# Kernel tuning notes

Measured on AMD Instinct MI355X. Metric: run time of the kernel, lower is better.

## Reference

```python
import jax, jax.numpy as jnp
import numpy as np

B, V, T, P, F, H = 256, 16, 64, 24, 8, 256
OUT = 4  # output_size


def setup_inputs() -> dict:
    key = jax.random.key(0)
    ks = jax.random.split(key, 8)
    s = 0.1
    return {
        "sequence": jax.random.uniform(ks[0], (B, V, T, F), dtype=jnp.float32),
        "dist_matrix": jax.random.uniform(ks[1], (B, V, V), dtype=jnp.float32),
        "rb_matrix": jax.random.uniform(ks[2], (B, V, V), dtype=jnp.float32),
        "cog_matrix": jax.random.uniform(ks[3], (B, V, V), dtype=jnp.float32),
        "seq_mask": jnp.ones((B, V, T), dtype=jnp.float32),
        "maxval": jnp.ones((B, F), dtype=jnp.float32),
        "minval": jnp.zeros((B, F), dtype=jnp.float32),
        # per-vessel distinct LSTMCell weights (torch gate order i,f,g,o)
        "W_ih": jax.random.normal(ks[4], (V, 4 * H, F), dtype=jnp.float32) * s,
        "W_hh": jax.random.normal(ks[5], (V, 4 * H, H), dtype=jnp.float32) * s,
        "b_ih": jnp.zeros((V, 4 * H), dtype=jnp.float32),
        "b_hh": jnp.zeros((V, 4 * H), dtype=jnp.float32),
        # per-vessel attention Linear(2H -> H)
        "W_att": jax.random.normal(ks[6], (V, H, 2 * H), dtype=jnp.float32) * s,
        "b_att": jnp.zeros((V, H), dtype=jnp.float32),
        # shared output Linear(H -> F)
        "W_out": jax.random.normal(ks[7], (F, H), dtype=jnp.float32) * s,
        "b_out": jnp.zeros((F,), dtype=jnp.float32),
        "maxVessels": V,
    }


def _lstm(x, h, c, W_ih, W_hh, b_ih, b_hh):
    # grouped LSTMCell over all vessels at once: x [B,V,F], h/c [B,V,H]
    gates = (jnp.einsum('bvf,vgf->bvg', x, W_ih) + b_ih
             + jnp.einsum('bvh,vgh->bvg', h, W_hh) + b_hh)
    i, f, g, o = jnp.split(gates, 4, axis=-1)
    c = jax.nn.sigmoid(f) * c + jax.nn.sigmoid(i) * jnp.tanh(g)
    h = jax.nn.sigmoid(o) * jnp.tanh(c)
    return h, c


def reference(sequence, dist_matrix, rb_matrix, cog_matrix, seq_mask, maxval, minval,
              W_ih, W_hh, b_ih, b_hh, W_att, b_att, W_out, b_out, maxVessels):
    B_, V_, T_, F_ = sequence.shape
    H_ = W_hh.shape[-1]
    mx = maxval[:, None, :]  # [B,1,F] -> broadcast to [B,V,F]
    mn = minval[:, None, :]

    # ---- encoder: scan over sequence_length, all vessels batched ----
    def enc_step(carry, x_t):
        h, c = carry
        h, c = _lstm(x_t, h, c, W_ih, W_hh, b_ih, b_hh)
        return (h, c), h

    h0 = jnp.zeros((B_, V_, H_), sequence.dtype)
    c0 = jnp.zeros((B_, V_, H_), sequence.dtype)
    (h, c), enc = jax.lax.scan(enc_step, (h0, c0), jnp.moveaxis(sequence, 2, 0))
    enc = jnp.moveaxis(enc, 0, 2)  # [B,V,T,H]

    # ---- decoder: scan over prediction_length ----
    def dec_step(carry, _):
        h, c, prev = carry
        # torch.tensor(x.data) detaches -> stop_gradient; then denormalize
        prev_seq = jax.lax.stop_gradient(prev) * (mx - mn) + mn
        # attention score: batched dot of encoder states with decoder hidden
        score = jnp.einsum('bvth,bvh->bvt', enc, h)
        alpha = jax.nn.softmax(score * seq_mask, axis=-1)
        cv = jnp.einsum('bvt,bvth->bvh', alpha, enc)  # context vector
        # faithful replication of torch.stack((cv, h)).view(B, 2H) per vessel
        cat = jnp.stack([cv, h], axis=0)              # [2,B,V,H]
        cat = cat.transpose(2, 0, 1, 3).reshape(V_, B_, 2 * H_)  # [V,B,2H]
        h_att = jnp.tanh(jnp.einsum('vbk,vhk->vbh', cat, W_att) + b_att[:, None, :])
        h_att = h_att.transpose(1, 0, 2)              # [B,V,H]
        h2, c2 = _lstm(prev_seq, h_att, c, W_ih, W_hh, b_ih, b_hh)
        out = jax.nn.relu(jnp.einsum('bvh,fh->bvf', h2, W_out) + b_out)
        return (h2, c2, out), out

    prev0 = sequence[:, :, -1, :]
    _, outs = jax.lax.scan(dec_step, (h, c, prev0), None, length=P)
    outs = jnp.moveaxis(outs, 0, 2)  # [B,V,P,F]
    return jnp.clip(outs[..., :OUT], 0.0, 1.0)
```

## Files before the change

kernel.cpp:

```cpp
#include <hip/hip_runtime.h>
#include <hip/hip_bf16.h>

namespace {

typedef unsigned short u16;
constexpr int B_ = 256, V_ = 16, T_ = 64, P_ = 24, F_ = 8, H_ = 256, G_ = 1024;

typedef __attribute__((ext_vector_type(8))) short bf16x8;
typedef __attribute__((ext_vector_type(4))) float f32x4;

__device__ __forceinline__ float sigm(float x) { return 1.0f / (1.0f + __expf(-x)); }
__device__ __forceinline__ float bf2f(u16 s) {
  union { unsigned u; float f; } x; x.u = ((unsigned)s) << 16; return x.f;
}
__device__ __forceinline__ u16 f2bf(float f) {
  union { float f; unsigned u; } x; x.f = f;
  unsigned r = x.u + 0x7fffu + ((x.u >> 16) & 1u);
  return (u16)(r >> 16);
}
__device__ __forceinline__ void split2(float w, u16& hi, u16& lo) {
  hi = f2bf(w);
  lo = f2bf(w - bf2f(hi));
}
__device__ __forceinline__ void load16(const void* g, void* l) {
  __builtin_amdgcn_global_load_lds(
      (const __attribute__((address_space(1))) unsigned*)g,
      (__attribute__((address_space(3))) unsigned*)l, 16, 0, 0);
}
__device__ __forceinline__ f32x4 mfma16(bf16x8 a, bf16x8 b, f32x4 c) {
  return __builtin_amdgcn_mfma_f32_16x16x32_bf16(a, b, c, 0, 0, 0);
}

__global__ void init_kernel(float* __restrict__ c, float* __restrict__ prev,
                            const float* __restrict__ seq) {
  int idx = blockIdx.x * 256 + threadIdx.x;
  if (idx < B_ * V_ * H_ / 4) ((float4*)c)[idx] = float4{0.f, 0.f, 0.f, 0.f};
  if (idx < B_ * V_ * F_ / 4) {
    int v = idx >> 9, rem = idx & 511;
    int b = rem >> 1, fq = rem & 1;
    ((float4*)prev)[idx] = ((const float4*)seq)[(((size_t)b * V_ + v) * T_ + (T_ - 1)) * 2 + fq];
  }
}

__global__ void convert_kernel(const float* __restrict__ Whh, const float* __restrict__ Watt,
                               u16* __restrict__ whhH, u16* __restrict__ whhL,
                               u16* __restrict__ wattH, u16* __restrict__ wattL) {
  int gid = blockIdx.x * 256 + threadIdx.x;
  const int n1 = V_ * G_ * H_ / 4;
  const int n2 = V_ * H_ * 2 * H_ / 4;
  const float* src; u16 *dH, *dL; int i;
  if (gid < n1)            { src = Whh;  dH = whhH;  dL = whhL;  i = gid; }
  else if (gid < n1 + n2)  { src = Watt; dH = wattH; dL = wattL; i = gid - n1; }
  else return;
  float4 wv = ((const float4*)src)[i];
  u16 h0,l0,h1,l1,h2,l2,h3,l3;
  split2(wv.x,h0,l0); split2(wv.y,h1,l1); split2(wv.z,h2,l2); split2(wv.w,h3,l3);
  uint2 oh; oh.x = (unsigned)h0 | ((unsigned)h1 << 16); oh.y = (unsigned)h2 | ((unsigned)h3 << 16);
  uint2 ol; ol.x = (unsigned)l0 | ((unsigned)l1 << 16); ol.y = (unsigned)l2 | ((unsigned)l3 << 16);
  ((uint2*)dH)[i] = oh; ((uint2*)dL)[i] = ol;
}

__global__ void copy_h_kernel(const u16* __restrict__ enc, const u16* __restrict__ hlo1,
                              u16* __restrict__ hdecHi, u16* __restrict__ hdecLo) {
  int gid = blockIdx.x * 256 + threadIdx.x;
  int row = gid >> 5, jq = gid & 31;
  ((uint4*)hdecHi)[gid] = ((const uint4*)enc)[((size_t)row * T_ + (T_ - 1)) * 32 + jq];
  ((uint4*)hdecLo)[gid] = ((const uint4*)hlo1)[gid];
}

template <int MODE>
__global__ __launch_bounds__(512) void lstm_mfma_kernel(
    const float* __restrict__ xin,
    u16* __restrict__ enc,
    const u16* __restrict__ hloIn,
    u16* __restrict__ hloOut,
    const u16* __restrict__ aHi,
    const u16* __restrict__ aLo,
    u16* __restrict__ hdecHi, u16* __restrict__ hdecLo,
    float* __restrict__ cbuf,
    const u16* __restrict__ WhhHi, const u16* __restrict__ WhhLo,
    const float* __restrict__ W_ih, const float* __restrict__ b_ih,
    const float* __restrict__ b_hh,
    const float* __restrict__ maxv, const float* __restrict__ minv,
    int t)
{
  __shared__ char smem[74240];
  float* xsf   = (float*)(smem + 65536);
  float* wisf  = (float*)(smem + 69632);
  float* bsumf = (float*)(smem + 73728);

  int bid = blockIdx.x;
  int xcd = bid & 7, idx = bid >> 3;
  int v  = xcd * 2 + (idx & 1);
  int bt = (idx >> 1) & 1;
  int ch = idx >> 2;
  int b0 = bt * 128, c0 = ch * 32;
  int tid = threadIdx.x, lane = tid & 63, w = tid >> 6;
  int wr = w >> 1, wc = w & 1;

  if (tid < 256) {
    int b_l = tid >> 1, fq = tid & 1;
    int b = b0 + b_l;
    float4 xv;
    if (MODE == 0) {
      xv = *(const float4*)(xin + (((size_t)b * V_ + v) * T_ + t) * F_ + fq * 4);
    } else {
      float4 pv = *(const float4*)(xin + ((size_t)v * B_ + b) * F_ + fq * 4);
      float4 mx = *(const float4*)(maxv + b * F_ + fq * 4);
      float4 mn = *(const float4*)(minv + b * F_ + fq * 4);
      xv.x = pv.x * (mx.x - mn.x) + mn.x;
      xv.y = pv.y * (mx.y - mn.y) + mn.y;
      xv.z = pv.z * (mx.z - mn.z) + mn.z;
      xv.w = pv.w * (mx.w - mn.w) + mn.w;
    }
    *(float4*)(xsf + b_l * 8 + fq * 4) = xv;
  } else {
    int idx2 = tid - 256;
    int gc = idx2 >> 1, half = idx2 & 1;
    int grow = ((gc >> 5) << 8) + c0 + (gc & 31);
    *(float4*)(wisf + gc * 8 + half * 4) =
        *(const float4*)(W_ih + ((size_t)v * G_ + grow) * F_ + half * 4);
  }
  if (tid < 128) {
    int grow = ((tid >> 5) << 8) + c0 + (tid & 31);
    bsumf[tid] = b_ih[v * G_ + grow] + b_hh[v * G_ + grow];
  }

  const bool hasK = (MODE == 1) || (t > 0);

  auto stageAB = [&](int ks, int bufn) {
    int kc = ks * 32;
    int row = tid >> 2, g2 = tid & 3;
    int kb = ((g2 ^ ((row >> 1) & 3)) << 4);
    size_t boff = ((((size_t)v * G_ + ((row >> 5) << 8) + c0 + (row & 31)) * H_ + kc) << 1) + kb;
    load16((const char*)WhhHi + boff, smem + 32768 + bufn * 8192 + tid * 16);
    load16((const char*)WhhLo + boff, smem + 49152 + bufn * 8192 + tid * 16);
    if (MODE == 0) {
      size_t offH = ((((size_t)(v * B_ + b0 + row)) * T_ + (t - 1)) * H_ + kc) * 2 + kb;
      size_t offL = (((size_t)(v * B_ + b0 + row)) * H_ + kc) * 2 + kb;
      load16((const char*)enc + offH,   smem + bufn * 8192 + tid * 16);
      load16((const char*)hloIn + offL, smem + 16384 + bufn * 8192 + tid * 16);
    } else {
      size_t offA = (((size_t)(v * B_ + b0 + row)) * H_ + kc) * 2 + kb;
      load16((const char*)aHi + offA, smem + bufn * 8192 + tid * 16);
      load16((const char*)aLo + offA, smem + 16384 + bufn * 8192 + tid * 16);
    }
  };

  f32x4 acc[2][4];
  #pragma unroll
  for (int i = 0; i < 2; ++i)
    #pragma unroll
    for (int g = 0; g < 4; ++g) acc[i][g] = f32x4{0.f, 0.f, 0.f, 0.f};

  if (hasK) stageAB(0, 0);
  __syncthreads();

  if (hasK) {
    int rA = lane & 15, kg = lane >> 4;
    int ar0 = wr * 32 + rA;
    int aoff0 = ar0 * 64 + ((kg ^ ((ar0 >> 1) & 3)) << 4);
    int br0 = wc * 16 + rA;
    int boff0 = br0 * 64 + ((kg ^ ((br0 >> 1) & 3)) << 4);
    int buf = 0;
    for (int ks = 0; ks < 8; ++ks) {
      if (ks < 7) stageAB(ks + 1, buf ^ 1);
      const char* Ah = smem + buf * 8192;
      const char* Al = smem + 16384 + buf * 8192;
      const char* Bh = smem + 32768 + buf * 8192;
      const char* Bl = smem + 49152 + buf * 8192;
      bf16x8 ah0 = *(const bf16x8*)(Ah + aoff0);
      bf16x8 ah1 = *(const bf16x8*)(Ah + aoff0 + 1024);
      bf16x8 al0 = *(const bf16x8*)(Al + aoff0);
      bf16x8 al1 = *(const bf16x8*)(Al + aoff0 + 1024);
      bf16x8 bh[4], bl[4];
      #pragma unroll
      for (int g = 0; g < 4; ++g) {
        bh[g] = *(const bf16x8*)(Bh + boff0 + g * 2048);
        bl[g] = *(const bf16x8*)(Bl + boff0 + g * 2048);
      }
      #pragma unroll
      for (int g = 0; g < 4; ++g) {
        acc[0][g] = mfma16(ah0, bh[g], acc[0][g]);
        acc[1][g] = mfma16(ah1, bh[g], acc[1][g]);
      }
      #pragma unroll
      for (int g = 0; g < 4; ++g) {
        acc[0][g] = mfma16(al0, bh[g], acc[0][g]);
        acc[1][g] = mfma16(al1, bh[g], acc[1][g]);
      }
      #pragma unroll
      for (int g = 0; g < 4; ++g) {
        acc[0][g] = mfma16(ah0, bl[g], acc[0][g]);
        acc[1][g] = mfma16(ah1, bl[g], acc[1][g]);
      }
      __syncthreads();
      buf ^= 1;
    }
  }

  {
    int rA = lane & 15;
    int cc = wc * 16 + rA;
    int col = c0 + cc;
    float bs[4], wr8[4][8];
    #pragma unroll
    for (int g = 0; g < 4; ++g) {
      int gc = g * 32 + cc;
      bs[g] = bsumf[gc];
      #pragma unroll
      for (int f = 0; f < 8; ++f) wr8[g][f] = wisf[gc * 8 + f];
    }
    int rowg = (lane >> 4) * 4;
    #pragma unroll
    for (int i = 0; i < 2; ++i) {
      #pragma unroll
      for (int r = 0; r < 4; ++r) {
        int b_l = wr * 32 + i * 16 + rowg + r;
        const float* xf = xsf + b_l * 8;
        float s[4];
        #pragma unroll
        for (int g = 0; g < 4; ++g) {
          float sv = acc[i][g][r] + bs[g];
          #pragma unroll
          for (int f = 0; f < 8; ++f) sv = fmaf(wr8[g][f], xf[f], sv);
          s[g] = sv;
        }
        size_t gidx = ((size_t)(v * B_ + b0 + b_l)) * H_ + col;
        float cold = cbuf[gidx];
        float cn = sigm(s[1]) * cold + sigm(s[0]) * tanhf(s[2]);
        float hn = sigm(s[3]) * tanhf(cn);
        cbuf[gidx] = cn;
        u16 hi, lo; split2(hn, hi, lo);
        if (MODE == 0) {
          enc[(((size_t)(v * B_ + b0 + b_l)) * T_ + t) * H_ + col] = hi;
          hloOut[gidx] = lo;
        } else {
          hdecHi[gidx] = hi;
          hdecLo[gidx] = lo;
        }
      }
    }
  }
}

__global__ __launch_bounds__(256) void attn_kernel(
    const u16* __restrict__ enc, const u16* __restrict__ hHi, const u16* __restrict__ hLo,
    const float* __restrict__ mask, u16* __restrict__ cvHi, u16* __restrict__ cvLo)
{
  __shared__ u16 et[T_ * H_];
  __shared__ float hh[H_];
  __shared__ float ss[T_];
  int bx = blockIdx.x;
  int v = bx >> 8, b = bx & 255;
  int tid = threadIdx.x;

  const char* erow = (const char*)(enc + ((size_t)(v * B_ + b)) * T_ * H_);
  #pragma unroll
  for (int it2 = 0; it2 < 8; ++it2) {
    int gidx = it2 * 256 + tid;
    load16(erow + gidx * 16, (char*)et + gidx * 16);
  }
  {
    size_t hidx = ((size_t)v * B_ + b) * H_ + tid;
    hh[tid] = bf2f(hHi[hidx]) + bf2f(hLo[hidx]);
  }
  __syncthreads();

  int t = tid >> 2, part = tid & 3;
  const u16* ep = et + t * H_ + part * 64;
  float acc = 0.f;
  #pragma unroll
  for (int it = 0; it < 8; ++it) {
    uint4 uu = *(const uint4*)(ep + it * 8);
    const float* hp = &hh[part * 64 + it * 8];
    acc = fmaf(bf2f((u16)(uu.x & 0xffff)), hp[0], acc);
    acc = fmaf(bf2f((u16)(uu.x >> 16)),    hp[1], acc);
    acc = fmaf(bf2f((u16)(uu.y & 0xffff)), hp[2], acc);
    acc = fmaf(bf2f((u16)(uu.y >> 16)),    hp[3], acc);
    acc = fmaf(bf2f((u16)(uu.z & 0xffff)), hp[4], acc);
    acc = fmaf(bf2f((u16)(uu.z >> 16)),    hp[5], acc);
    acc = fmaf(bf2f((u16)(uu.w & 0xffff)), hp[6], acc);
    acc = fmaf(bf2f((u16)(uu.w >> 16)),    hp[7], acc);
  }
  acc += __shfl_xor(acc, 1, 64);
  acc += __shfl_xor(acc, 2, 64);
  if (part == 0) ss[t] = acc * mask[((size_t)b * V_ + v) * T_ + t];
  __syncthreads();

  if (tid < 64) {
    float s = ss[tid];
    float m = s;
    #pragma unroll
    for (int d = 32; d >= 1; d >>= 1) m = fmaxf(m, __shfl_xor(m, d, 64));
    float e = __expf(s - m);
    float se = e;
    #pragma unroll
    for (int d = 32; d >= 1; d >>= 1) se += __shfl_xor(se, d, 64);
    ss[tid] = e / se;
  }
  __syncthreads();

  int j = tid;
  float a = 0.f;
  #pragma unroll 8
  for (int tt = 0; tt < T_; ++tt)
    a = fmaf(ss[tt], bf2f(et[tt * H_ + j]), a);
  u16 hi, lo; split2(a, hi, lo);
  size_t cidx = ((size_t)v * B_ + b) * H_ + j;
  cvHi[cidx] = hi;
  cvLo[cidx] = lo;
}

__global__ __launch_bounds__(256) void attg_mfma_kernel(
    const u16* __restrict__ cvHi, const u16* __restrict__ cvLo,
    const u16* __restrict__ hdHi, const u16* __restrict__ hdLo,
    const u16* __restrict__ WattHi, const u16* __restrict__ WattLo,
    const float* __restrict__ b_att,
    u16* __restrict__ hattHi, u16* __restrict__ hattLo)
{
  __shared__ char smem[40960];
  int bx = blockIdx.x;
  int v = bx >> 4, bt = (bx >> 1) & 7, nh = bx & 1;
  int bp0 = bt * 32, n0 = nh * 128;
  int tid = threadIdx.x, lane = tid & 63, w = tid >> 6;

  auto stageAB = [&](int ks, int bufn) {
    int kc = ks * 32;
    #pragma unroll
    for (int it = 0; it < 2; ++it) {
      int gb = it * 256 + tid;
      int nl = gb >> 2, g2 = gb & 3;
      int kb = ((g2 ^ ((nl >> 1) & 3)) << 4);
      size_t off = ((((size_t)v * H_ + n0 + nl) * (2 * H_) + kc) << 1) + kb;
      load16((const char*)WattHi + off, smem + 8192  + bufn * 8192 + gb * 16);
      load16((const char*)WattLo + off, smem + 24576 + bufn * 8192 + gb * 16);
    }
    {
      int g = tid & 127;
      int b = g >> 2, g2 = g & 3;
      int kb = ((g2 ^ ((b >> 1) & 3)) << 4);
      int bp = bp0 + b;
      const u16* baseH = (bp < 128) ? (cvHi + ((size_t)v * B_ + 2 * bp) * H_)
                                    : (hdHi + ((size_t)v * B_ + 2 * (bp - 128)) * H_);
      const u16* baseL = (bp < 128) ? (cvLo + ((size_t)v * B_ + 2 * bp) * H_)
                                    : (hdLo + ((size_t)v * B_ + 2 * (bp - 128)) * H_);
      if (tid < 128) load16((const char*)baseH + kc * 2 + kb, smem + bufn * 2048 + g * 16);
      else           load16((const char*)baseL + kc * 2 + kb, smem + 4096 + bufn * 2048 + g * 16);
    }
  };

  f32x4 acc[2][2];
  #pragma unroll
  for (int i = 0; i < 2; ++i)
    #pragma unroll
    for (int j = 0; j < 2; ++j) acc[i][j] = f32x4{0.f, 0.f, 0.f, 0.f};

  stageAB(0, 0);
  __syncthreads();

  int rA = lane & 15, kg = lane >> 4;
  int aoff0 = rA * 64 + ((kg ^ ((rA >> 1) & 3)) << 4);
  int gc0 = w * 32 + rA;
  int boff0 = gc0 * 64 + ((kg ^ ((gc0 >> 1) & 3)) << 4);
  int buf = 0;
  for (int ks = 0; ks < 16; ++ks) {
    if (ks < 15) stageAB(ks + 1, buf ^ 1);
    const char* Ah = smem + buf * 2048;
    const char* Al = smem + 4096  + buf * 2048;
    const char* Bh = smem + 8192  + buf * 8192;
    const char* Bl = smem + 24576 + buf * 8192;
    bf16x8 ah0 = *(const bf16x8*)(Ah + aoff0);
    bf16x8 ah1 = *(const bf16x8*)(Ah + aoff0 + 1024);
    bf16x8 al0 = *(const bf16x8*)(Al + aoff0);
    bf16x8 al1 = *(const bf16x8*)(Al + aoff0 + 1024);
    bf16x8 bh0 = *(const bf16x8*)(Bh + boff0);
    bf16x8 bh1 = *(const bf16x8*)(Bh + boff0 + 1024);
    bf16x8 bl0 = *(const bf16x8*)(Bl + boff0);
    bf16x8 bl1 = *(const bf16x8*)(Bl + boff0 + 1024);
    acc[0][0] = mfma16(ah0, bh0, acc[0][0]);
    acc[0][1] = mfma16(ah0, bh1, acc[0][1]);
    acc[1][0] = mfma16(ah1, bh0, acc[1][0]);
    acc[1][1] = mfma16(ah1, bh1, acc[1][1]);
    acc[0][0] = mfma16(al0, bh0, acc[0][0]);
    acc[0][1] = mfma16(al0, bh1, acc[0][1]);
    acc[1][0] = mfma16(al1, bh0, acc[1][0]);
    acc[1][1] = mfma16(al1, bh1, acc[1][1]);
    acc[0][0] = mfma16(ah0, bl0, acc[0][0]);
    acc[0][1] = mfma16(ah0, bl1, acc[0][1]);
    acc[1][0] = mfma16(ah1, bl0, acc[1][0]);
    acc[1][1] = mfma16(ah1, bl1, acc[1][1]);
    __syncthreads();
    buf ^= 1;
  }

  int rowg = (lane >> 4) * 4;
  #pragma unroll
  for (int i = 0; i < 2; ++i)
    #pragma unroll
    for (int j = 0; j < 2; ++j) {
      int n = n0 + w * 32 + j * 16 + rA;
      float bias = b_att[v * H_ + n];
      #pragma unroll
      for (int r = 0; r < 4; ++r) {
        int bp = bp0 + i * 16 + rowg + r;
        float tv = tanhf(acc[i][j][r] + bias);
        u16 hi, lo; split2(tv, hi, lo);
        size_t hidx = ((size_t)v * B_ + bp) * H_ + n;
        hattHi[hidx] = hi;
        hattLo[hidx] = lo;
      }
    }
}

__global__ __launch_bounds__(256) void out_kernel(
    const u16* __restrict__ hHi, const u16* __restrict__ hLo,
    const float* __restrict__ W_out, const float* __restrict__ b_out,
    float* __restrict__ prev, float* __restrict__ out, int p)
{
  int gid = blockIdx.x * 256 + threadIdx.x;
  int row = gid >> 3;
  int f = gid & 7;
  int v = row >> 8, b = row & 255;
  const u16* hp = hHi + (size_t)row * H_;
  const u16* lp = hLo + (size_t)row * H_;
  const float* wp = W_out + f * H_;
  float acc = 0.f;
  #pragma unroll 4
  for (int k = 0; k < H_; k += 8) {
    uint4 hv = *(const uint4*)(hp + k);
    uint4 lv = *(const uint4*)(lp + k);
    float4 w0 = *(const float4*)(wp + k);
    float4 w1 = *(const float4*)(wp + k + 4);
    acc = fmaf(bf2f((u16)(hv.x & 0xffff)) + bf2f((u16)(lv.x & 0xffff)), w0.x, acc);
    acc = fmaf(bf2f((u16)(hv.x >> 16))    + bf2f((u16)(lv.x >> 16)),    w0.y, acc);
    acc = fmaf(bf2f((u16)(hv.y & 0xffff)) + bf2f((u16)(lv.y & 0xffff)), w0.z, acc);
    acc = fmaf(bf2f((u16)(hv.y >> 16))    + bf2f((u16)(lv.y >> 16)),    w0.w, acc);
    acc = fmaf(bf2f((u16)(hv.z & 0xffff)) + bf2f((u16)(lv.z & 0xffff)), w1.x, acc);
    acc = fmaf(bf2f((u16)(hv.z >> 16))    + bf2f((u16)(lv.z >> 16)),    w1.y, acc);
    acc = fmaf(bf2f((u16)(hv.w & 0xffff)) + bf2f((u16)(lv.w & 0xffff)), w1.z, acc);
    acc = fmaf(bf2f((u16)(hv.w >> 16))    + bf2f((u16)(lv.w >> 16)),    w1.w, acc);
  }
  float o = fmaxf(acc + b_out[f], 0.f);
  prev[gid] = o;
  if (f < 4)
    out[(((size_t)b * V_ + v) * P_ + p) * 4 + f] = fminf(o, 1.f);
}

}

extern "C" void kernel_launch(void* const* d_in, const int* in_sizes, int n_in,
                              void* d_out, int out_size, void* d_ws, size_t ws_size,
                              hipStream_t stream)
{
  const float* seq   = (const float*)d_in[0];
  const float* smask = (const float*)d_in[4];
  const float* maxv  = (const float*)d_in[5];
  const float* minv  = (const float*)d_in[6];
  const float* W_ih  = (const float*)d_in[7];
  const float* W_hh  = (const float*)d_in[8];
  const float* b_ih  = (const float*)d_in[9];
  const float* b_hh  = (const float*)d_in[10];
  const float* W_att = (const float*)d_in[11];
  const float* b_att = (const float*)d_in[12];
  const float* W_out = (const float*)d_in[13];
  const float* b_out = (const float*)d_in[14];
  float* out = (float*)d_out;

  char* ws = (char*)d_ws;
  float* c     = (float*)(ws);
  float* prev  = (float*)(ws + 4194304);
  u16* h_lo    = (u16*)(ws + 4325376);
  u16* hdecHi  = (u16*)(ws + 8519680);
  u16* hdecLo  = (u16*)(ws + 10616832);
  u16* hattHi  = (u16*)(ws + 12713984);
  u16* hattLo  = (u16*)(ws + 14811136);
  u16* cvHi    = (u16*)(ws + 16908288);
  u16* cvLo    = (u16*)(ws + 19005440);
  u16* whhHi   = (u16*)(ws + 21102592);
  u16* whhLo   = (u16*)(ws + 29491200);
  u16* wattHi  = (u16*)(ws + 37879808);
  u16* wattLo  = (u16*)(ws + 42074112);
  u16* enc     = (u16*)(ws + 46268416);

  const size_t SZ = (size_t)V_ * B_ * H_;

  init_kernel<<<1024, 256, 0, stream>>>(c, prev, seq);
  convert_kernel<<<6144, 256, 0, stream>>>(W_hh, W_att, whhHi, whhLo, wattHi, wattLo);

  for (int t = 0; t < T_; ++t) {
    lstm_mfma_kernel<0><<<256, 512, 0, stream>>>(seq, enc,
        h_lo + ((t + 1) & 1) * SZ, h_lo + (t & 1) * SZ,
        nullptr, nullptr, nullptr, nullptr, c, whhHi, whhLo,
        W_ih, b_ih, b_hh, nullptr, nullptr, t);
  }
  copy_h_kernel<<<512, 256, 0, stream>>>(enc, h_lo + SZ, hdecHi, hdecLo);

  for (int p = 0; p < P_; ++p) {
    attn_kernel<<<V_ * B_, 256, 0, stream>>>(enc, hdecHi, hdecLo, smask, cvHi, cvLo);
    attg_mfma_kernel<<<256, 256, 0, stream>>>(cvHi, cvLo, hdecHi, hdecLo,
        wattHi, wattLo, b_att, hattHi, hattLo);
    lstm_mfma_kernel<1><<<256, 512, 0, stream>>>(prev, nullptr, nullptr, nullptr,
        hattHi, hattLo, hdecHi, hdecLo, c, whhHi, whhLo,
        W_ih, b_ih, b_hh, maxv, minv, 1);
    out_kernel<<<128, 256, 0, stream>>>(hdecHi, hdecLo, W_out, b_out, prev, out, p);
  }
}
```

Before: 2.628 ms.

## Replace per-timestep encoder LSTM launches with persistent cooperative kernel

The 64 per-timestep encoder LSTM launches become one cooperative persistent kernel that runs all timesteps and uses grid.sync between them. Each block loads its slice of the split-bf16 W_hh into shared memory once and keeps it there for all steps. W_ih, the summed bias and the cell state stay in registers and c is written out only at the end. This removes launch overhead and the repeated weight and cell-state traffic, at the cost of about 148KB of LDS per block and a grid-wide barrier every step, and it needs all 256 blocks to be co-resident.

```diff
diff --git a/kernel.cpp b/kernel.cpp
--- a/kernel.cpp
+++ b/kernel.cpp
@@ -1,5 +1,8 @@
 #include <hip/hip_runtime.h>
 #include <hip/hip_bf16.h>
+#include <hip/hip_cooperative_groups.h>
+
+namespace cg = cooperative_groups;
 
 namespace {
 
@@ -66,6 +69,155 @@
   int row = gid >> 5, jq = gid & 31;
   ((uint4*)hdecHi)[gid] = ((const uint4*)enc)[((size_t)row * T_ + (T_ - 1)) * 32 + jq];
   ((uint4*)hdecLo)[gid] = ((const uint4*)hlo1)[gid];
+}
+
+__global__ __launch_bounds__(512) void enc_persist_kernel(
+    const float* __restrict__ seq,
+    u16* __restrict__ enc,
+    u16* __restrict__ h_lo,
+    float* __restrict__ cbuf,
+    const u16* __restrict__ WhhHi, const u16* __restrict__ WhhLo,
+    const float* __restrict__ W_ih, const float* __restrict__ b_ih,
+    const float* __restrict__ b_hh)
+{
+  __shared__ char smem[151552];
+  float* xsf = (float*)(smem + 147456);
+
+  cg::grid_group grid = cg::this_grid();
+
+  int bid = blockIdx.x;
+  int v  = (bid & 7) * 2 + ((bid >> 3) & 1);
+  int bt = (bid >> 4) & 1;
+  int ch = bid >> 5;
+  int b0 = bt * 128, c0 = ch * 32;
+  int tid = threadIdx.x, lane = tid & 63, w = tid >> 6;
+  int wr = w >> 1, wc = w & 1;
+  int rA = lane & 15, kg = lane >> 4;
+  int rowg = (lane >> 4) * 4;
+  int cc = wc * 16 + rA;
+  int col = c0 + cc;
+
+  #pragma unroll
+  for (int it = 0; it < 8; ++it) {
+    int gidx = it * 512 + tid;
+    int row = gidx >> 5, gsub = gidx & 31;
+    int chunk = gsub >> 2, g2 = gsub & 3;
+    int grow = ((row >> 5) << 8) + c0 + (row & 31);
+    size_t off = ((((size_t)v * G_ + grow) * H_ + chunk * 32) << 1)
+               + ((g2 ^ ((row >> 1) & 3)) << 4);
+    load16((const char*)WhhHi + off, smem + gidx * 16);
+    load16((const char*)WhhLo + off, smem + 65536 + gidx * 16);
+  }
+
+  float wih[4][8], bs[4];
+  #pragma unroll
+  for (int g = 0; g < 4; ++g) {
+    int grow = (g << 8) + col;
+    #pragma unroll
+    for (int f = 0; f < 8; ++f) wih[g][f] = W_ih[((size_t)v * G_ + grow) * F_ + f];
+    bs[g] = b_ih[v * G_ + grow] + b_hh[v * G_ + grow];
+  }
+
+  float creg[2][4];
+  #pragma unroll
+  for (int i = 0; i < 2; ++i)
+    #pragma unroll
+    for (int r = 0; r < 4; ++r) creg[i][r] = 0.f;
+
+  int ar0 = wr * 32 + rA;
+  int aoff0 = ar0 * 64 + ((kg ^ ((ar0 >> 1) & 3)) << 4);
+  int brow[4], bxor[4];
+  #pragma unroll
+  for (int g = 0; g < 4; ++g) {
+    int rowb = cc + g * 32;
+    brow[g] = rowb * 512;
+    bxor[g] = ((kg ^ ((rowb >> 1) & 3)) << 4);
+  }
+
+  const size_t SZ = (size_t)V_ * B_ * H_;
+
+  for (int t = 0; t < T_; ++t) {
+    if (tid < 256) {
+      int b_l = tid >> 1, fq = tid & 1;
+      int b = b0 + b_l;
+      float4 xv = *(const float4*)(seq + (((size_t)b * V_ + v) * T_ + t) * F_ + fq * 4);
+      *(float4*)(xsf + b_l * 8 + fq * 4) = xv;
+    }
+
+    f32x4 acc[2][4];
+    #pragma unroll
+    for (int i = 0; i < 2; ++i)
+      #pragma unroll
+      for (int g = 0; g < 4; ++g) acc[i][g] = f32x4{0.f, 0.f, 0.f, 0.f};
+
+    if (t > 0) {
+      const u16* hloPrev = h_lo + ((t + 1) & 1) * SZ;
+      for (int ks = 0; ks < 8; ++ks) {
+        {
+          int row = tid >> 2, g2 = tid & 3;
+          int kb = ((g2 ^ ((row >> 1) & 3)) << 4);
+          size_t offH = ((((size_t)(v * B_ + b0 + row)) * T_ + (t - 1)) * H_ + ks * 32) * 2 + kb;
+          size_t offL = (((size_t)(v * B_ + b0 + row)) * H_ + ks * 32) * 2 + kb;
+          load16((const char*)enc + offH,     smem + 131072 + tid * 16);
+          load16((const char*)hloPrev + offL, smem + 139264 + tid * 16);
+        }
+        __syncthreads();
+        const char* Ah = smem + 131072;
+        const char* Al = smem + 139264;
+        bf16x8 ah0 = *(const bf16x8*)(Ah + aoff0);
+        bf16x8 ah1 = *(const bf16x8*)(Ah + aoff0 + 1024);
+        bf16x8 al0 = *(const bf16x8*)(Al + aoff0);
+        bf16x8 al1 = *(const bf16x8*)(Al + aoff0 + 1024);
+        #pragma unroll
+        for (int g = 0; g < 4; ++g) {
+          bf16x8 bh = *(const bf16x8*)(smem + brow[g] + ks * 64 + bxor[g]);
+          bf16x8 bl = *(const bf16x8*)(smem + 65536 + brow[g] + ks * 64 + bxor[g]);
+          acc[0][g] = mfma16(ah0, bh, acc[0][g]);
+          acc[1][g] = mfma16(ah1, bh, acc[1][g]);
+          acc[0][g] = mfma16(al0, bh, acc[0][g]);
+          acc[1][g] = mfma16(al1, bh, acc[1][g]);
+          acc[0][g] = mfma16(ah0, bl, acc[0][g]);
+          acc[1][g] = mfma16(ah1, bl, acc[1][g]);
+        }
+        __syncthreads();
+      }
+    } else {
+      __syncthreads();
+    }
+
+    u16* hloCur = h_lo + (t & 1) * SZ;
+    #pragma unroll
+    for (int i = 0; i < 2; ++i) {
+      #pragma unroll
+      for (int r = 0; r < 4; ++r) {
+        int b_l = wr * 32 + i * 16 + rowg + r;
+        const float* xf = xsf + b_l * 8;
+        float s[4];
+        #pragma unroll
+        for (int g = 0; g < 4; ++g) {
+          float sv = acc[i][g][r] + bs[g];
+          #pragma unroll
+          for (int f = 0; f < 8; ++f) sv = fmaf(wih[g][f], xf[f], sv);
+          s[g] = sv;
+        }
+        float cn = sigm(s[1]) * creg[i][r] + sigm(s[0]) * tanhf(s[2]);
+        float hn = sigm(s[3]) * tanhf(cn);
+        creg[i][r] = cn;
+        u16 hi, lo; split2(hn, hi, lo);
+        enc[(((size_t)(v * B_ + b0 + b_l)) * T_ + t) * H_ + col] = hi;
+        hloCur[((size_t)(v * B_ + b0 + b_l)) * H_ + col] = lo;
+      }
+    }
+    grid.sync();
+  }
+
+  #pragma unroll
+  for (int i = 0; i < 2; ++i)
+    #pragma unroll
+    for (int r = 0; r < 4; ++r) {
+      int b_l = wr * 32 + i * 16 + rowg + r;
+      cbuf[((size_t)(v * B_ + b0 + b_l)) * H_ + col] = creg[i][r];
+    }
 }
 
 template <int MODE>
@@ -483,18 +635,19 @@
   u16* wattLo  = (u16*)(ws + 42074112);
   u16* enc     = (u16*)(ws + 46268416);
 
-  const size_t SZ = (size_t)V_ * B_ * H_;
-
   init_kernel<<<1024, 256, 0, stream>>>(c, prev, seq);
   convert_kernel<<<6144, 256, 0, stream>>>(W_hh, W_att, whhHi, whhLo, wattHi, wattLo);
 
-  for (int t = 0; t < T_; ++t) {
-    lstm_mfma_kernel<0><<<256, 512, 0, stream>>>(seq, enc,
-        h_lo + ((t + 1) & 1) * SZ, h_lo + (t & 1) * SZ,
-        nullptr, nullptr, nullptr, nullptr, c, whhHi, whhLo,
-        W_ih, b_ih, b_hh, nullptr, nullptr, t);
-  }
-  copy_h_kernel<<<512, 256, 0, stream>>>(enc, h_lo + SZ, hdecHi, hdecLo);
+  {
+    void* args[] = {
+      (void*)&seq, (void*)&enc, (void*)&h_lo, (void*)&c,
+      (void*)&whhHi, (void*)&whhLo, (void*)&W_ih, (void*)&b_ih, (void*)&b_hh
+    };
+    hipLaunchCooperativeKernel((const void*)enc_persist_kernel,
+                               dim3(256), dim3(512), args, 0, stream);
+  }
+
+  copy_h_kernel<<<512, 256, 0, stream>>>(enc, h_lo + (size_t)V_ * B_ * H_, hdecHi, hdecLo);
 
   for (int p = 0; p < P_; ++p) {
     attn_kernel<<<V_ * B_, 256, 0, stream>>>(enc, hdecHi, hdecLo, smask, cvHi, cvLo);
```

After: 4.484 ms. 70.7% more time.
